# Kernel optimization log

Measured on AMD Instinct MI355X. Metric: run time of the kernel, lower is better.

## Reference

```python
import jax, jax.numpy as jnp
import numpy as np

BITS = 4
PACK = 32 // BITS  # 8 nibbles per int32
MASK = (1 << BITS) - 1  # 0xF, maxq for 4-bit


def _unpack_rows(q):
    # q: [K//PACK, N] int32, nibbles packed along the input (row) dim
    shifts = (jnp.arange(PACK, dtype=jnp.int32) * BITS)
    vals = (q[:, None, :] >> shifts[None, :, None]) & MASK  # [K//PACK, PACK, N]
    return vals.reshape(q.shape[0] * PACK, q.shape[1])      # [K, N]


def _unpack_cols(q):
    # q: [1, N//PACK] int32, nibbles packed along the output (col) dim
    shifts = (jnp.arange(PACK, dtype=jnp.int32) * BITS)
    vals = (q[:, :, None] >> shifts[None, None, :]) & MASK  # [1, N//PACK, PACK]
    return vals.reshape(q.shape[0], q.shape[1] * PACK)       # [1, N]


def setup_inputs() -> dict:
    key = jax.random.key(0)
    k1, k2, k3, k4 = jax.random.split(key, 4)
    M, K, N = 4096, 4096, 11008
    x = jax.random.normal(k1, (M, K), dtype=jnp.float16)
    qweight = jax.random.randint(k2, (K // PACK, N), jnp.iinfo(jnp.int32).min,
                                 jnp.iinfo(jnp.int32).max, dtype=jnp.int32)
    qzeros = jax.random.randint(k3, (1, N // PACK), jnp.iinfo(jnp.int32).min,
                                jnp.iinfo(jnp.int32).max, dtype=jnp.int32)
    # realistic small positive per-channel scales
    scales = (jax.random.uniform(k4, (1, N), dtype=jnp.float32) * 0.01 + 1e-3).astype(jnp.float16)
    return {"x": x, "qweight": qweight, "qzeros": qzeros, "scales": scales}


def reference(x, qweight, qzeros, scales):
    # GPTQ/exllama 4-bit dequant: w = scale * (q - (zero + 1)), single group
    wq = _unpack_rows(qweight)                      # [K, N] int32 in [0, 15]
    zeros = _unpack_cols(qzeros) + 1                # [1, N] int32
    w = (wq - zeros).astype(jnp.float16) * scales   # [K, N] fp16
    out = jnp.dot(x, w)                             # [M, N] fp16 GEMM
    return out
```

## Files before the change

kernel.cpp:

```cpp
#include <hip/hip_runtime.h>
#include <stdint.h>

#define M_DIM 4096
#define K_DIM 4096
#define N_DIM 11008

typedef _Float16 half2v __attribute__((ext_vector_type(2)));
typedef _Float16 half8  __attribute__((ext_vector_type(8)));
typedef float    f32x4  __attribute__((ext_vector_type(4)));

#define SCHED_FENCE() __builtin_amdgcn_sched_barrier(0)

__device__ __forceinline__ unsigned int pkrtz_bits(float a, float b) {
  typedef __fp16 fp16x2 __attribute__((ext_vector_type(2)));
  union { fp16x2 h; unsigned int u; } c;
  c.h = __builtin_amdgcn_cvt_pkrtz(a, b);
  return c.u;
}

__device__ __forceinline__ half8 pack8(float4 lo, float4 hi) {
  union { unsigned int u[4]; half8 v; } r;
  r.u[0] = pkrtz_bits(lo.x, hi.x);
  r.u[1] = pkrtz_bits(lo.y, hi.y);
  r.u[2] = pkrtz_bits(lo.z, hi.z);
  r.u[3] = pkrtz_bits(lo.w, hi.w);
  return r.v;
}

__global__ __launch_bounds__(256) void convert_x(const float* __restrict__ X,
                                                 _Float16* __restrict__ X16) {
  size_t g = (size_t)blockIdx.x * 256 + threadIdx.x;
  const float4* p = (const float4*)(X + g * 8);
  float4 lo = p[0], hi = p[1];
  *(half8*)(X16 + g * 8) = pack8(lo, hi);
}

__device__ __forceinline__ half8 unpack8(unsigned int q, half2v zoff) {
  union { unsigned int u; half2v h; } t0, t1, t2, t3;
  t0.u = (q & 0x000F000Fu) | 0x64006400u;
  t1.u = ((q >> 4) & 0x000F000Fu) | 0x64006400u;
  t2.u = ((q >> 8) & 0x000F000Fu) | 0x64006400u;
  t3.u = ((q >> 12) & 0x000F000Fu) | 0x64006400u;
  union { half2v h[4]; half8 v; } r;
  r.h[0] = t0.h - zoff;
  r.h[1] = t1.h - zoff;
  r.h[2] = t2.h - zoff;
  r.h[3] = t3.h - zoff;
  return r.v;
}

__device__ __forceinline__ void stage16(const void* g, void* l) {
  __builtin_amdgcn_global_load_lds((__attribute__((address_space(1))) unsigned int*)g,
                                   (__attribute__((address_space(3))) unsigned int*)l,
                                   16, 0, 0);
}

__global__ __launch_bounds__(256, 3) void gptq_gemm(
    const _Float16* __restrict__ X16,
    const int* __restrict__ QW,
    const int* __restrict__ QZ,
    const float* __restrict__ SC,
    float* __restrict__ OUT) {
  const int tid  = threadIdx.x;
  const int lane = tid & 63;
  const int wave = tid >> 6;
  const int wr   = wave >> 1;
  const int wc   = wave & 1;
  const int quad = lane >> 4;
  const int l16  = lane & 15;
  const int bx = blockIdx.x;
  const int by = blockIdx.y;

  __shared__ __align__(16) _Float16 ldsA[3 * 1024 * 8];

  const _Float16* gA = X16 + (size_t)(by * 128 + (tid & 127)) * K_DIM + (tid >> 7) * 8;
  _Float16* lw = ldsA + (size_t)tid * 8;

  const int* qp = QW + (size_t)quad * N_DIM + bx * 128 + wc * 64 + l16;

  half2v zoff[4];
  float sc[4];
#pragma unroll
  for (int nt = 0; nt < 4; ++nt) {
    int n = bx * 128 + wc * 64 + nt * 16 + l16;
    int z = (QZ[n >> 3] >> ((n & 7) * 4)) & 15;
    union { unsigned int u; half2v h; } zc;
    unsigned int zb = 0x6400u + (unsigned int)(z + 1);
    zc.u = (zb << 16) | zb;
    zoff[nt] = zc.h;
    sc[nt] = SC[n];
  }

  f32x4 acc[4][4] = {};

  int q0[2][4], q1[2][4];
#pragma unroll
  for (int i = 0; i < 4; ++i)
    stage16(gA + i * 16, lw + i * 2048);
  SCHED_FENCE();
#pragma unroll
  for (int s = 0; s < 2; ++s)
#pragma unroll
    for (int nt = 0; nt < 4; ++nt)
      q0[s][nt] = qp[(s * 4) * N_DIM + nt * 16];
  SCHED_FENCE();
  gA += 64;
  qp += 8 * N_DIM;
#pragma unroll
  for (int i = 0; i < 4; ++i)
    stage16(gA + i * 16, lw + 8192 + i * 2048);
  SCHED_FENCE();
#pragma unroll
  for (int s = 0; s < 2; ++s)
#pragma unroll
    for (int nt = 0; nt < 4; ++nt)
      q1[s][nt] = qp[(s * 4) * N_DIM + nt * 16];
  SCHED_FENCE();
  asm volatile("s_waitcnt vmcnt(12)" ::: "memory");
  __builtin_amdgcn_s_barrier();

  int rb = 0;
  int wb = 2;
  for (int ks = 0; ks < 64; ++ks) {
    int nq[2][4];
    if (ks < 62) {
      gA += 64;
      qp += 8 * N_DIM;
      _Float16* lb = ldsA + wb * 8192 + (size_t)tid * 8;
#pragma unroll
      for (int i = 0; i < 4; ++i)
        stage16(gA + i * 16, lb + i * 2048);
#pragma unroll
      for (int s = 0; s < 2; ++s)
#pragma unroll
        for (int nt = 0; nt < 4; ++nt)
          nq[s][nt] = qp[(s * 4) * N_DIM + nt * 16];
      SCHED_FENCE();
    }

    const _Float16* base = ldsA + rb * 8192;
#pragma unroll
    for (int s = 0; s < 2; ++s) {
      half8 a[4];
#pragma unroll
      for (int mt = 0; mt < 4; ++mt)
        a[mt] = *(const half8*)(base + ((s * 4 + quad) * 128 + wr * 64 + mt * 16 + l16) * 8);
      half8 b[4];
#pragma unroll
      for (int nt = 0; nt < 4; ++nt)
        b[nt] = unpack8((unsigned int)q0[s][nt], zoff[nt]);
      __builtin_amdgcn_s_setprio(1);
#pragma unroll
      for (int mt = 0; mt < 4; ++mt)
#pragma unroll
        for (int nt = 0; nt < 4; ++nt)
          acc[mt][nt] = __builtin_amdgcn_mfma_f32_16x16x32_f16(a[mt], b[nt], acc[mt][nt], 0, 0, 0);
      __builtin_amdgcn_s_setprio(0);
    }

#pragma unroll
    for (int s = 0; s < 2; ++s)
#pragma unroll
      for (int nt = 0; nt < 4; ++nt) {
        q0[s][nt] = q1[s][nt];
        if (ks < 62) q1[s][nt] = nq[s][nt];
      }
    rb = (rb == 2) ? 0 : rb + 1;
    wb = (wb == 2) ? 0 : wb + 1;

    if (ks < 63) {
      SCHED_FENCE();
      if (ks < 62)
        asm volatile("s_waitcnt vmcnt(12)" ::: "memory");
      else
        asm volatile("s_waitcnt vmcnt(0)" ::: "memory");
      __builtin_amdgcn_s_barrier();
    }
  }

#pragma unroll
  for (int mt = 0; mt < 4; ++mt) {
    int mbase = by * 128 + wr * 64 + mt * 16 + quad * 4;
#pragma unroll
    for (int nt = 0; nt < 4; ++nt) {
      int n = bx * 128 + wc * 64 + nt * 16 + l16;
      float s = sc[nt];
#pragma unroll
      for (int pp = 0; pp < 4; ++pp)
        OUT[(size_t)(mbase + pp) * N_DIM + n] = acc[mt][nt][pp] * s;
    }
  }
}

extern "C" void kernel_launch(void* const* d_in, const int* in_sizes, int n_in,
                              void* d_out, int out_size, void* d_ws, size_t ws_size,
                              hipStream_t stream) {
  const float* X  = (const float*)d_in[0];
  const int* QW   = (const int*)d_in[1];
  const int* QZ   = (const int*)d_in[2];
  const float* SC = (const float*)d_in[3];
  float* OUT      = (float*)d_out;
  _Float16* X16   = (_Float16*)d_ws;

  convert_x<<<dim3((M_DIM * (size_t)K_DIM / 8) / 256), 256, 0, stream>>>(X, X16);
  dim3 grid(N_DIM / 128, M_DIM / 128);
  gptq_gemm<<<grid, 256, 0, stream>>>(X16, QW, QZ, SC, OUT);
}
```

Before: 643.5 us.

## Switch to 32x32x16 MFMA with 256x128 block tile and K-step 32

Replaces the 16x16x32 MFMA tiling with 32x32x16 MFMA instructions and doubles the block tile along M to 256 rows, while halving the K step per iteration to 32. Each wave now computes a 128x64 output tile using 8 accumulators of 16 floats, so each unpacked weight fragment is reused across more rows and LDS reads per FLOP drop. The weight-dequantisation work per block is amortised over twice as many rows. In exchange, occupancy falls to 2 blocks per CU, the loop runs twice as many iterations with more barriers, and each block holds more accumulator registers.

After: 719.1 us. 11.8% more time.

```diff
diff --git a/kernel.cpp b/kernel.cpp
--- a/kernel.cpp
+++ b/kernel.cpp
@@ -7,7 +7,7 @@
 
 typedef _Float16 half2v __attribute__((ext_vector_type(2)));
 typedef _Float16 half8  __attribute__((ext_vector_type(8)));
-typedef float    f32x4  __attribute__((ext_vector_type(4)));
+typedef float    f32x16 __attribute__((ext_vector_type(16)));
 
 #define SCHED_FENCE() __builtin_amdgcn_sched_barrier(0)
 
@@ -55,7 +55,7 @@
                                    16, 0, 0);
 }
 
-__global__ __launch_bounds__(256, 3) void gptq_gemm(
+__global__ __launch_bounds__(256, 2) void gptq_gemm(
     const _Float16* __restrict__ X16,
     const int* __restrict__ QW,
     const int* __restrict__ QZ,
@@ -66,23 +66,21 @@
   const int wave = tid >> 6;
   const int wr   = wave >> 1;
   const int wc   = wave & 1;
-  const int quad = lane >> 4;
-  const int l16  = lane & 15;
+  const int l32  = lane & 31;
+  const int kh   = lane >> 5;
   const int bx = blockIdx.x;
   const int by = blockIdx.y;
 
-  __shared__ __align__(16) _Float16 ldsA[3 * 1024 * 8];
-
-  const _Float16* gA = X16 + (size_t)(by * 128 + (tid & 127)) * K_DIM + (tid >> 7) * 8;
-  _Float16* lw = ldsA + (size_t)tid * 8;
-
-  const int* qp = QW + (size_t)quad * N_DIM + bx * 128 + wc * 64 + l16;
-
-  half2v zoff[4];
-  float sc[4];
-#pragma unroll
-  for (int nt = 0; nt < 4; ++nt) {
-    int n = bx * 128 + wc * 64 + nt * 16 + l16;
+  __shared__ __align__(16) _Float16 ldsA[3 * 8192];
+
+  const _Float16* gA = X16 + (size_t)(by * 256 + tid) * K_DIM;
+  const int* qB = QW + (size_t)kh * N_DIM + bx * 128 + wc * 64 + l32;
+
+  half2v zoff[2];
+  float sc[2];
+#pragma unroll
+  for (int nt = 0; nt < 2; ++nt) {
+    int n = bx * 128 + wc * 64 + nt * 32 + l32;
     int z = (QZ[n >> 3] >> ((n & 7) * 4)) & 15;
     union { unsigned int u; half2v h; } zc;
     unsigned int zb = 0x6400u + (unsigned int)(z + 1);
@@ -91,87 +89,90 @@
     sc[nt] = SC[n];
   }
 
-  f32x4 acc[4][4] = {};
-
-  int q0[2][4], q1[2][4];
-#pragma unroll
-  for (int i = 0; i < 4; ++i)
-    stage16(gA + i * 16, lw + i * 2048);
-  SCHED_FENCE();
-#pragma unroll
-  for (int s = 0; s < 2; ++s)
-#pragma unroll
-    for (int nt = 0; nt < 4; ++nt)
-      q0[s][nt] = qp[(s * 4) * N_DIM + nt * 16];
-  SCHED_FENCE();
-  gA += 64;
-  qp += 8 * N_DIM;
-#pragma unroll
-  for (int i = 0; i < 4; ++i)
-    stage16(gA + i * 16, lw + 8192 + i * 2048);
-  SCHED_FENCE();
-#pragma unroll
-  for (int s = 0; s < 2; ++s)
-#pragma unroll
-    for (int nt = 0; nt < 4; ++nt)
-      q1[s][nt] = qp[(s * 4) * N_DIM + nt * 16];
-  SCHED_FENCE();
-  asm volatile("s_waitcnt vmcnt(12)" ::: "memory");
+  f32x16 acc[4][2] = {};
+  int q0[2][2], q1[2][2];
+
+  {
+    _Float16* lb = ldsA + (size_t)tid * 8;
+#pragma unroll
+    for (int i = 0; i < 4; ++i)
+      stage16(gA + i * 8, lb + i * 2048);
+#pragma unroll
+    for (int s = 0; s < 2; ++s)
+#pragma unroll
+      for (int nt = 0; nt < 2; ++nt)
+        q0[s][nt] = qB[(size_t)(s * 2) * N_DIM + nt * 32];
+    SCHED_FENCE();
+#pragma unroll
+    for (int i = 0; i < 4; ++i)
+      stage16(gA + 32 + i * 8, lb + 8192 + i * 2048);
+#pragma unroll
+    for (int s = 0; s < 2; ++s)
+#pragma unroll
+      for (int nt = 0; nt < 2; ++nt)
+        q1[s][nt] = qB[(size_t)(4 + s * 2) * N_DIM + nt * 32];
+    SCHED_FENCE();
+  }
+  gA += 32;
+  qB += (size_t)4 * N_DIM;
+  asm volatile("s_waitcnt vmcnt(8)" ::: "memory");
   __builtin_amdgcn_s_barrier();
 
   int rb = 0;
   int wb = 2;
-  for (int ks = 0; ks < 64; ++ks) {
-    int nq[2][4];
-    if (ks < 62) {
-      gA += 64;
-      qp += 8 * N_DIM;
+  for (int ks = 0; ks < 128; ++ks) {
+    int nq[2][2];
+    if (ks < 126) {
+      gA += 32;
+      qB += (size_t)4 * N_DIM;
       _Float16* lb = ldsA + wb * 8192 + (size_t)tid * 8;
 #pragma unroll
       for (int i = 0; i < 4; ++i)
-        stage16(gA + i * 16, lb + i * 2048);
+        stage16(gA + i * 8, lb + i * 2048);
 #pragma unroll
       for (int s = 0; s < 2; ++s)
 #pragma unroll
-        for (int nt = 0; nt < 4; ++nt)
-          nq[s][nt] = qp[(s * 4) * N_DIM + nt * 16];
+        for (int nt = 0; nt < 2; ++nt)
+          nq[s][nt] = qB[(size_t)(s * 2) * N_DIM + nt * 32];
       SCHED_FENCE();
     }
 
     const _Float16* base = ldsA + rb * 8192;
 #pragma unroll
     for (int s = 0; s < 2; ++s) {
-      half8 a[4];
-#pragma unroll
-      for (int mt = 0; mt < 4; ++mt)
-        a[mt] = *(const half8*)(base + ((s * 4 + quad) * 128 + wr * 64 + mt * 16 + l16) * 8);
-      half8 b[4];
-#pragma unroll
-      for (int nt = 0; nt < 4; ++nt)
-        b[nt] = unpack8((unsigned int)q0[s][nt], zoff[nt]);
+      const _Float16* ab = base + (size_t)((s * 2 + kh) * 256 + wr * 128 + l32) * 8;
+      half8 a0 = *(const half8*)(ab);
+      half8 a1 = *(const half8*)(ab + 32 * 8);
+      half8 a2 = *(const half8*)(ab + 64 * 8);
+      half8 a3 = *(const half8*)(ab + 96 * 8);
+      half8 b0 = unpack8((unsigned int)q0[s][0], zoff[0]);
+      half8 b1 = unpack8((unsigned int)q0[s][1], zoff[1]);
       __builtin_amdgcn_s_setprio(1);
-#pragma unroll
-      for (int mt = 0; mt < 4; ++mt)
-#pragma unroll
-        for (int nt = 0; nt < 4; ++nt)
-          acc[mt][nt] = __builtin_amdgcn_mfma_f32_16x16x32_f16(a[mt], b[nt], acc[mt][nt], 0, 0, 0);
+      acc[0][0] = __builtin_amdgcn_mfma_f32_32x32x16_f16(a0, b0, acc[0][0], 0, 0, 0);
+      acc[0][1] = __builtin_amdgcn_mfma_f32_32x32x16_f16(a0, b1, acc[0][1], 0, 0, 0);
+      acc[1][0] = __builtin_amdgcn_mfma_f32_32x32x16_f16(a1, b0, acc[1][0], 0, 0, 0);
+      acc[1][1] = __builtin_amdgcn_mfma_f32_32x32x16_f16(a1, b1, acc[1][1], 0, 0, 0);
+      acc[2][0] = __builtin_amdgcn_mfma_f32_32x32x16_f16(a2, b0, acc[2][0], 0, 0, 0);
+      acc[2][1] = __builtin_amdgcn_mfma_f32_32x32x16_f16(a2, b1, acc[2][1], 0, 0, 0);
+      acc[3][0] = __builtin_amdgcn_mfma_f32_32x32x16_f16(a3, b0, acc[3][0], 0, 0, 0);
+      acc[3][1] = __builtin_amdgcn_mfma_f32_32x32x16_f16(a3, b1, acc[3][1], 0, 0, 0);
       __builtin_amdgcn_s_setprio(0);
     }
 
 #pragma unroll
     for (int s = 0; s < 2; ++s)
 #pragma unroll
-      for (int nt = 0; nt < 4; ++nt) {
+      for (int nt = 0; nt < 2; ++nt) {
         q0[s][nt] = q1[s][nt];
-        if (ks < 62) q1[s][nt] = nq[s][nt];
+        if (ks < 126) q1[s][nt] = nq[s][nt];
       }
     rb = (rb == 2) ? 0 : rb + 1;
     wb = (wb == 2) ? 0 : wb + 1;
 
-    if (ks < 63) {
+    if (ks < 127) {
       SCHED_FENCE();
-      if (ks < 62)
-        asm volatile("s_waitcnt vmcnt(12)" ::: "memory");
+      if (ks < 126)
+        asm volatile("s_waitcnt vmcnt(8)" ::: "memory");
       else
         asm volatile("s_waitcnt vmcnt(0)" ::: "memory");
       __builtin_amdgcn_s_barrier();
@@ -180,14 +181,16 @@
 
 #pragma unroll
   for (int mt = 0; mt < 4; ++mt) {
-    int mbase = by * 128 + wr * 64 + mt * 16 + quad * 4;
-#pragma unroll
-    for (int nt = 0; nt < 4; ++nt) {
-      int n = bx * 128 + wc * 64 + nt * 16 + l16;
-      float s = sc[nt];
-#pragma unroll
-      for (int pp = 0; pp < 4; ++pp)
-        OUT[(size_t)(mbase + pp) * N_DIM + n] = acc[mt][nt][pp] * s;
+#pragma unroll
+    for (int nt = 0; nt < 2; ++nt) {
+      const int n = bx * 128 + wc * 64 + nt * 32 + l32;
+      const float s = sc[nt];
+      const size_t mb = (size_t)(by * 256 + wr * 128 + mt * 32 + kh * 4);
+#pragma unroll
+      for (int r = 0; r < 16; ++r) {
+        const int row = (r & 3) + 8 * (r >> 2);
+        OUT[(mb + row) * N_DIM + n] = acc[mt][nt][r] * s;
+      }
     }
   }
 }
@@ -203,6 +206,6 @@
   _Float16* X16   = (_Float16*)d_ws;
 
   convert_x<<<dim3((M_DIM * (size_t)K_DIM / 8) / 256), 256, 0, stream>>>(X, X16);
-  dim3 grid(N_DIM / 128, M_DIM / 128);
+  dim3 grid(N_DIM / 128, M_DIM / 256);
   gptq_gemm<<<grid, 256, 0, stream>>>(X16, QW, QZ, SC, OUT);
 }
```
